# Kernel optimization log

Measured on AMD Instinct MI355X. Metric: run time of the kernel, lower is better.

Reference implementation:

```python
import jax, jax.numpy as jnp
import numpy as np

B, H, S, D = 4, 16, 4096, 64

def setup_inputs() -> dict:
    key = jax.random.key(0)
    kq, kk, kv = jax.random.split(key, 3)
    q = jax.random.normal(kq, (B, H, S, D), dtype=jnp.float32)
    k = jax.random.normal(kk, (B, H, S, D), dtype=jnp.float32)
    v = jax.random.normal(kv, (B, H, S, D), dtype=jnp.float32)
    return {"q": q, "k": k, "v": v}

def reference(q, k, v):
    # Original: (q @ k^T) @ v with score [B,H,S,S].
    # Mathematically identical reassociation: q @ (k^T @ v),
    # state kv has shape [B,H,D,D] -> avoids the SxS intermediate.
    kv = jnp.einsum('bhsd,bhse->bhde', k, v)  # [B,H,D,D]
    out = jnp.einsum('bhsd,bhde->bhse', q, kv)  # [B,H,S,D]
    return out
```

## Files before the change

### kernel.cpp

```cpp
#include <hip/hip_runtime.h>

#define BH  64
#define SEQ 4096
#define DH  64
#define KTILE 32
#define NCHUNK 16

__device__ __forceinline__ void gload_lds16(const float* g, float* l) {
  __builtin_amdgcn_global_load_lds(
      (const __attribute__((address_space(1))) void*)g,
      (__attribute__((address_space(3))) void*)l, 16, 0, 0);
}

__global__ __launch_bounds__(256) void kv_partial_kernel(
    const float* __restrict__ k, const float* __restrict__ v,
    float* __restrict__ partial, int rows_per_chunk) {
  const int t = threadIdx.x;
  const int bh = blockIdx.x >> 4;
  const int chunk = blockIdx.x & (NCHUNK - 1);

  const float* kb = k + (size_t)bh * SEQ * DH + (size_t)chunk * rows_per_chunk * DH;
  const float* vb = v + (size_t)bh * SEQ * DH + (size_t)chunk * rows_per_chunk * DH;

  __shared__ float smem[8192];

  const int g    = t & 63;
  const int grp  = t >> 6;
  const int d0 = (g & 7) * 8;
  const int e0 = (g >> 3) * 8;

  float acc[8][8];
#pragma unroll
  for (int i = 0; i < 8; ++i)
#pragma unroll
    for (int j = 0; j < 8; ++j) acc[i][j] = 0.f;

  const int ntiles = rows_per_chunk / KTILE;

  auto STAGE = [&](int tt, int b) {
    const float* ksrc = kb + (size_t)tt * KTILE * DH;
    const float* vsrc = vb + (size_t)tt * KTILE * DH;
    float* kd = smem + b * 2048;
    float* vd = smem + 4096 + b * 2048;
    const int wo = grp * 512;
    gload_lds16(ksrc + wo + g * 4,       kd + wo);
    gload_lds16(ksrc + wo + 256 + g * 4, kd + wo + 256);
    gload_lds16(vsrc + wo + g * 4,       vd + wo);
    gload_lds16(vsrc + wo + 256 + g * 4, vd + wo + 256);
  };

  STAGE(0, 0);
  asm volatile("s_waitcnt vmcnt(0)" ::: "memory");
  __syncthreads();

  int cur = 0;
  for (int tt = 0; tt < ntiles; ++tt) {
    if (tt + 1 < ntiles) STAGE(tt + 1, cur ^ 1);

    const float* ksb = smem + cur * 2048;
    const float* vsb = smem + 4096 + cur * 2048;
#pragma unroll
    for (int rr = 0; rr < 8; ++rr) {
      const int r = grp * 8 + rr;
      float4 ka0 = *(const float4*)&ksb[r * 64 + d0];
      float4 ka1 = *(const float4*)&ksb[r * 64 + d0 + 4];
      float4 va0 = *(const float4*)&vsb[r * 64 + e0];
      float4 va1 = *(const float4*)&vsb[r * 64 + e0 + 4];
      float kk[8] = {ka0.x, ka0.y, ka0.z, ka0.w, ka1.x, ka1.y, ka1.z, ka1.w};
      float vv[8] = {va0.x, va0.y, va0.z, va0.w, va1.x, va1.y, va1.z, va1.w};
#pragma unroll
      for (int i = 0; i < 8; ++i)
#pragma unroll
        for (int j = 0; j < 8; ++j) acc[i][j] += kk[i] * vv[j];
    }

    asm volatile("s_waitcnt vmcnt(0)" ::: "memory");
    __syncthreads();
    cur ^= 1;
  }

  if (grp >= 2) {
    float* reg = smem + (grp - 2) * 4096;
#pragma unroll
    for (int i = 0; i < 8; ++i) {
      float4 w0 = {acc[i][0], acc[i][1], acc[i][2], acc[i][3]};
      float4 w1 = {acc[i][4], acc[i][5], acc[i][6], acc[i][7]};
      *(float4*)&reg[(2 * i) * 256 + g * 4]     = w0;
      *(float4*)&reg[(2 * i + 1) * 256 + g * 4] = w1;
    }
  }
  __syncthreads();
  if (grp < 2) {
    const float* reg = smem + grp * 4096;
#pragma unroll
    for (int i = 0; i < 8; ++i) {
      float4 a = *(const float4*)&reg[(2 * i) * 256 + g * 4];
      float4 b = *(const float4*)&reg[(2 * i + 1) * 256 + g * 4];
      acc[i][0] += a.x; acc[i][1] += a.y; acc[i][2] += a.z; acc[i][3] += a.w;
      acc[i][4] += b.x; acc[i][5] += b.y; acc[i][6] += b.z; acc[i][7] += b.w;
    }
  }
  __syncthreads();
  if (grp == 1) {
#pragma unroll
    for (int i = 0; i < 8; ++i) {
      float4 w0 = {acc[i][0], acc[i][1], acc[i][2], acc[i][3]};
      float4 w1 = {acc[i][4], acc[i][5], acc[i][6], acc[i][7]};
      *(float4*)&smem[(2 * i) * 256 + g * 4]     = w0;
      *(float4*)&smem[(2 * i + 1) * 256 + g * 4] = w1;
    }
  }
  __syncthreads();
  if (grp == 0) {
#pragma unroll
    for (int i = 0; i < 8; ++i) {
      float4 a = *(const float4*)&smem[(2 * i) * 256 + g * 4];
      float4 b = *(const float4*)&smem[(2 * i + 1) * 256 + g * 4];
      acc[i][0] += a.x; acc[i][1] += a.y; acc[i][2] += a.z; acc[i][3] += a.w;
      acc[i][4] += b.x; acc[i][5] += b.y; acc[i][6] += b.z; acc[i][7] += b.w;
    }
    float* pb = partial + (size_t)blockIdx.x * (DH * DH);
#pragma unroll
    for (int i = 0; i < 8; ++i) {
      float4 w0 = {acc[i][0], acc[i][1], acc[i][2], acc[i][3]};
      float4 w1 = {acc[i][4], acc[i][5], acc[i][6], acc[i][7]};
      *(float4*)&pb[(d0 + i) * 64 + e0]     = w0;
      *(float4*)&pb[(d0 + i) * 64 + e0 + 4] = w1;
    }
  }
}

__global__ __launch_bounds__(256) void kv_reduce_kernel(
    const float* __restrict__ partial, float* __restrict__ kvf) {
  const int gid = blockIdx.x * 256 + threadIdx.x;
  const int bh = gid >> 10;
  const int idx = gid & 1023;
  float4 s = {0.f, 0.f, 0.f, 0.f};
  for (int c = 0; c < NCHUNK; ++c) {
    const float4* p = (const float4*)(partial + ((size_t)bh * NCHUNK + c) * (DH * DH));
    float4 x = p[idx];
    s.x += x.x; s.y += x.y; s.z += x.z; s.w += x.w;
  }
  ((float4*)kvf)[gid] = s;
}

__global__ __launch_bounds__(256) void out_kernel(
    const float* __restrict__ q, const float* __restrict__ kvf,
    float* __restrict__ out) {
  const int t = threadIdx.x;
  const int bh = blockIdx.x >> 6;
  const int rb = blockIdx.x & 63;
  const int row = rb * 64 + (t >> 2);
  const int c0 = (t & 3) * 16;

  __shared__ float kv_lds[64 * 64];

  const float4* gkv4 = (const float4*)(kvf + (size_t)bh * (DH * DH));
  float4* kv4 = (float4*)kv_lds;
#pragma unroll
  for (int j = 0; j < 4; ++j) kv4[t + j * 256] = gkv4[t + j * 256];

  const float* qrow = q + (size_t)bh * SEQ * DH + (size_t)row * DH;
  float4 qv[16];
#pragma unroll
  for (int i = 0; i < 16; ++i) qv[i] = *(const float4*)&qrow[i * 4];

  __syncthreads();

  float acc[16];
#pragma unroll
  for (int j = 0; j < 16; ++j) acc[j] = 0.f;

#pragma unroll
  for (int dc = 0; dc < 16; ++dc) {
    float qs[4] = {qv[dc].x, qv[dc].y, qv[dc].z, qv[dc].w};
#pragma unroll
    for (int dd = 0; dd < 4; ++dd) {
      const float* kr = &kv_lds[(dc * 4 + dd) * 64 + c0];
      float4 k0 = *(const float4*)&kr[0];
      float4 k1 = *(const float4*)&kr[4];
      float4 k2 = *(const float4*)&kr[8];
      float4 k3 = *(const float4*)&kr[12];
      const float qsv = qs[dd];
      acc[0]  += qsv * k0.x; acc[1]  += qsv * k0.y;
      acc[2]  += qsv * k0.z; acc[3]  += qsv * k0.w;
      acc[4]  += qsv * k1.x; acc[5]  += qsv * k1.y;
      acc[6]  += qsv * k1.z; acc[7]  += qsv * k1.w;
      acc[8]  += qsv * k2.x; acc[9]  += qsv * k2.y;
      acc[10] += qsv * k2.z; acc[11] += qsv * k2.w;
      acc[12] += qsv * k3.x; acc[13] += qsv * k3.y;
      acc[14] += qsv * k3.z; acc[15] += qsv * k3.w;
    }
  }

  float* ob = out + (size_t)bh * SEQ * DH + (size_t)row * DH + c0;
#pragma unroll
  for (int j = 0; j < 4; ++j) {
    float4 w = {acc[4 * j + 0], acc[4 * j + 1], acc[4 * j + 2], acc[4 * j + 3]};
    *(float4*)&ob[4 * j] = w;
  }
}

extern "C" void kernel_launch(void* const* d_in, const int* in_sizes, int n_in,
                              void* d_out, int out_size, void* d_ws, size_t ws_size,
                              hipStream_t stream) {
  const float* q = (const float*)d_in[0];
  const float* k = (const float*)d_in[1];
  const float* v = (const float*)d_in[2];
  float* out = (float*)d_out;

  float* kvf = (float*)d_ws;
  float* partial = kvf + (size_t)BH * DH * DH;

  const int rows = SEQ / NCHUNK;

  hipLaunchKernelGGL(kv_partial_kernel, dim3(BH * NCHUNK), dim3(256), 0, stream,
                     k, v, partial, rows);
  hipLaunchKernelGGL(kv_reduce_kernel, dim3(256), dim3(256), 0, stream,
                     partial, kvf);
  hipLaunchKernelGGL(out_kernel, dim3(BH * 64), dim3(256), 0, stream,
                     q, kvf, out);
}
```

Before: 90.35 us.

## Deepen kv_partial LDS pipeline to four buffers with smaller tiles

```diff
diff --git a/kernel.cpp b/kernel.cpp
--- a/kernel.cpp
+++ b/kernel.cpp
@@ -3,8 +3,10 @@
 #define BH  64
 #define SEQ 4096
 #define DH  64
-#define KTILE 32
 #define NCHUNK 16
+#define KTILE  16
+#define NT     16
+#define NBUF   4
 
 __device__ __forceinline__ void gload_lds16(const float* g, float* l) {
   __builtin_amdgcn_global_load_lds(
@@ -14,18 +16,18 @@
 
 __global__ __launch_bounds__(256) void kv_partial_kernel(
     const float* __restrict__ k, const float* __restrict__ v,
-    float* __restrict__ partial, int rows_per_chunk) {
+    float* __restrict__ partial) {
   const int t = threadIdx.x;
   const int bh = blockIdx.x >> 4;
   const int chunk = blockIdx.x & (NCHUNK - 1);
 
-  const float* kb = k + (size_t)bh * SEQ * DH + (size_t)chunk * rows_per_chunk * DH;
-  const float* vb = v + (size_t)bh * SEQ * DH + (size_t)chunk * rows_per_chunk * DH;
+  const float* kb = k + (size_t)bh * SEQ * DH + (size_t)chunk * (SEQ / NCHUNK) * DH;
+  const float* vb = v + (size_t)bh * SEQ * DH + (size_t)chunk * (SEQ / NCHUNK) * DH;
 
   __shared__ float smem[8192];
 
-  const int g    = t & 63;
-  const int grp  = t >> 6;
+  const int g   = t & 63;
+  const int grp = t >> 6;
   const int d0 = (g & 7) * 8;
   const int e0 = (g >> 3) * 8;
 
@@ -35,33 +37,21 @@
 #pragma unroll
     for (int j = 0; j < 8; ++j) acc[i][j] = 0.f;
 
-  const int ntiles = rows_per_chunk / KTILE;
-
-  auto STAGE = [&](int tt, int b) {
-    const float* ksrc = kb + (size_t)tt * KTILE * DH;
-    const float* vsrc = vb + (size_t)tt * KTILE * DH;
-    float* kd = smem + b * 2048;
-    float* vd = smem + 4096 + b * 2048;
-    const int wo = grp * 512;
-    gload_lds16(ksrc + wo + g * 4,       kd + wo);
-    gload_lds16(ksrc + wo + 256 + g * 4, kd + wo + 256);
-    gload_lds16(vsrc + wo + g * 4,       vd + wo);
-    gload_lds16(vsrc + wo + 256 + g * 4, vd + wo + 256);
+  auto STAGE = [&](int tt) {
+    const int buf = tt & (NBUF - 1);
+    const int wo = grp * 256;
+    const float* ksrc = kb + (size_t)tt * (KTILE * DH) + wo + g * 4;
+    const float* vsrc = vb + (size_t)tt * (KTILE * DH) + wo + g * 4;
+    gload_lds16(ksrc, smem + buf * 1024 + wo);
+    gload_lds16(vsrc, smem + 4096 + buf * 1024 + wo);
   };
 
-  STAGE(0, 0);
-  asm volatile("s_waitcnt vmcnt(0)" ::: "memory");
-  __syncthreads();
-
-  int cur = 0;
-  for (int tt = 0; tt < ntiles; ++tt) {
-    if (tt + 1 < ntiles) STAGE(tt + 1, cur ^ 1);
-
-    const float* ksb = smem + cur * 2048;
-    const float* vsb = smem + 4096 + cur * 2048;
-#pragma unroll
-    for (int rr = 0; rr < 8; ++rr) {
-      const int r = grp * 8 + rr;
+  auto COMPUTE = [&](int tt) {
+    const float* ksb = smem + (tt & (NBUF - 1)) * 1024;
+    const float* vsb = smem + 4096 + (tt & (NBUF - 1)) * 1024;
+#pragma unroll
+    for (int rr = 0; rr < 4; ++rr) {
+      const int r = grp * 4 + rr;
       float4 ka0 = *(const float4*)&ksb[r * 64 + d0];
       float4 ka1 = *(const float4*)&ksb[r * 64 + d0 + 4];
       float4 va0 = *(const float4*)&vsb[r * 64 + e0];
@@ -73,11 +63,27 @@
 #pragma unroll
         for (int j = 0; j < 8; ++j) acc[i][j] += kk[i] * vv[j];
     }
-
-    asm volatile("s_waitcnt vmcnt(0)" ::: "memory");
-    __syncthreads();
-    cur ^= 1;
-  }
+  };
+
+  STAGE(0); STAGE(1); STAGE(2);
+
+  for (int tt = 0; tt < NT - 2; ++tt) {
+    asm volatile("s_waitcnt vmcnt(4)" ::: "memory");
+    __builtin_amdgcn_s_barrier();
+    __builtin_amdgcn_sched_barrier(0);
+    if (tt + 3 < NT) STAGE(tt + 3);
+    COMPUTE(tt);
+  }
+  asm volatile("s_waitcnt vmcnt(2)" ::: "memory");
+  __builtin_amdgcn_s_barrier();
+  __builtin_amdgcn_sched_barrier(0);
+  COMPUTE(NT - 2);
+  asm volatile("s_waitcnt vmcnt(0)" ::: "memory");
+  __builtin_amdgcn_s_barrier();
+  __builtin_amdgcn_sched_barrier(0);
+  COMPUTE(NT - 1);
+
+  __syncthreads();
 
   if (grp >= 2) {
     float* reg = smem + (grp - 2) * 4096;
@@ -212,10 +218,8 @@
   float* kvf = (float*)d_ws;
   float* partial = kvf + (size_t)BH * DH * DH;
 
-  const int rows = SEQ / NCHUNK;
-
   hipLaunchKernelGGL(kv_partial_kernel, dim3(BH * NCHUNK), dim3(256), 0, stream,
-                     k, v, partial, rows);
+                     k, v, partial);
   hipLaunchKernelGGL(kv_reduce_kernel, dim3(256), dim3(256), 0, stream,
                      partial, kvf);
   hipLaunchKernelGGL(out_kernel, dim3(BH * 64), dim3(256), 0, stream,
```

After: 94.10 us. 1.04x slower.
